# Optimization experiments

Measured on AMD Instinct MI355X. Metric: run time of the kernel, lower is better.

The kernel has to match this reference:

```python
import jax, jax.numpy as jnp
import numpy as np

B, S, E = 4, 2048, 1024


def setup_inputs() -> dict:
    key = jax.random.key(0)
    ks = jax.random.split(key, 7)
    s = 1.0 / np.sqrt(E)  # torch Linear default init scale (uniform bound)
    inp = {
        "input": jax.random.normal(ks[0], (B, S, E), dtype=jnp.float32),
        "masked": 1,
        "W_q": jax.random.uniform(ks[1], (E, E), jnp.float32, -s, s),
        "b_q": jax.random.uniform(ks[2], (E,), jnp.float32, -s, s),
        "W_k": jax.random.uniform(ks[3], (E, E), jnp.float32, -s, s),
        "b_k": jax.random.uniform(ks[4], (E,), jnp.float32, -s, s),
        "W_v": jax.random.uniform(ks[5], (E, E), jnp.float32, -s, s),
        "b_v": jax.random.uniform(ks[6], (E,), jnp.float32, -s, s),
    }
    return inp


def reference(input, masked, W_q, b_q, W_k, b_k, W_v, b_v):
    # torch.nn.Linear: y = x @ W.T + b
    q = jnp.einsum("bse,fe->bsf", input, W_q) + b_q
    k = jnp.einsum("bse,fe->bsf", input, W_k) + b_k
    v = jnp.einsum("bse,fe->bsf", input, W_v) + b_v
    d = q.shape[-1]
    scores = jnp.einsum("bqd,bkd->bqk", q, k) / jnp.sqrt(jnp.float32(d))
    if masked:
        Sq = scores.shape[1]
        causal = jnp.tril(jnp.ones((Sq, Sq), dtype=bool))  # [S,S], broadcast over batch
        scores = jnp.where(causal, scores, -jnp.inf)
    attn = jax.nn.softmax(scores, axis=-1)
    return jnp.einsum("bqk,bkd->bqd", attn, v)
```

## Files before the change

kernel.cpp:

```cpp
#include <hip/hip_runtime.h>

typedef _Float16 f16;
typedef f16 f16x8 __attribute__((ext_vector_type(8)));
typedef f16 f16x4v __attribute__((ext_vector_type(4)));
typedef f16 f16x2v __attribute__((ext_vector_type(2)));
typedef float f32x4 __attribute__((ext_vector_type(4)));

__device__ __forceinline__ void async_ld16(const void* g, void* l) {
    __builtin_amdgcn_global_load_lds(
        (const __attribute__((address_space(1))) unsigned int*)g,
        (__attribute__((address_space(3))) unsigned int*)l, 16, 0, 0);
}

#define VMC(n) asm volatile("s_waitcnt vmcnt(" #n ")" ::: "memory")
#define BAR __builtin_amdgcn_s_barrier()


#define SSTG_A(b, kh, tOff) do {                                                \
    char* d_ = (char*)smem + (b) * 32768 + (kh) * 8192 + stgBase;               \
    async_ld16(pA  + (tOff) * 64 + (kh) * 32, d_);                              \
    async_ld16(pA1 + (tOff) * 64 + (kh) * 32, d_ + 4096);                       \
} while (0)
#define SSTG_B(b, kh, tOff) do {                                                \
    char* d_ = (char*)smem + (b) * 32768 + 16384 + (kh) * 8192 + stgBase;       \
    async_ld16(pB  + (tOff) * 64 + (kh) * 32, d_);                              \
    async_ld16(pB1 + (tOff) * 64 + (kh) * 32, d_ + 4096);                       \
} while (0)
#define SRD(b, kk) do {                                                         \
    const char* sa_ = (const char*)smem + (b) * 32768 + (kk) * 8192 + aOff;     \
    _Pragma("unroll") for (int m_ = 0; m_ < 4; ++m_)                            \
        af[m_] = *(const f16x8*)(sa_ + m_ * 1024);                              \
    const char* sb_ = (const char*)smem + (b) * 32768 + 16384 + (kk) * 8192 + bOff; \
    _Pragma("unroll") for (int n_ = 0; n_ < 4; ++n_)                            \
        bf[n_] = *(const f16x8*)(sb_ + n_ * 1024);                              \
} while (0)
#define SFENCE do {                                                             \
    __builtin_amdgcn_s_barrier();                                               \
    asm volatile("s_waitcnt lgkmcnt(0)" ::: "memory");                          \
    __builtin_amdgcn_sched_barrier(0);                                          \
    __builtin_amdgcn_s_setprio(1);                                              \
    _Pragma("unroll") for (int m_ = 0; m_ < 4; ++m_)                            \
        _Pragma("unroll") for (int n_ = 0; n_ < 4; ++n_)                        \
            acc[m_][n_] = __builtin_amdgcn_mfma_f32_16x16x32_f16(af[m_], bf[n_], acc[m_][n_], 0, 0, 0); \
    __builtin_amdgcn_s_setprio(0);                                              \
} while (0)

__global__ __launch_bounds__(256, 2) void scores128(
    const f16* __restrict__ Q, const f16* __restrict__ K,
    f16* __restrict__ P, const int* __restrict__ maskedp)
{
    const int masked = *maskedp;
    const int bx = blockIdx.x, by = blockIdx.y, bz = blockIdx.z;
    if (masked && bx > by) return;
    const int mBase = by * 128, nBase = bx * 128;
    const bool diag = (masked != 0) && (bx == by);

    __shared__ __align__(16) f16 smem[32768];
    const int tid = threadIdx.x;
    const int wave = tid >> 6, lane = tid & 63;
    const int wrow = wave >> 1, wcol = wave & 1;
    const int quad = lane >> 4, l16 = lane & 15;
    const int rowLane = tid >> 2;
    const int cOff = ((tid & 3) ^ ((tid >> 3) & 3)) * 8;
    const int stgBase = wave * 1024;
    const int swz  = (quad ^ ((l16 >> 1) & 3)) * 16;
    const int aOff = (wrow * 64 + l16) * 64 + swz;
    const int bOff = (wcol * 64 + l16) * 64 + swz;

    const f16* Ab = Q + (long)bz * (2048L * 1024);
    const f16* Bb = K + (long)bz * (2048L * 1024);
    const f16* pA  = Ab + (long)(mBase + rowLane) * 1024 + cOff;
    const f16* pA1 = pA + 64 * 1024;
    const f16* pB  = Bb + (long)(nBase + rowLane) * 1024 + cOff;
    const f16* pB1 = pB + 64 * 1024;

    f32x4 acc[4][4];
#pragma unroll
    for (int m = 0; m < 4; ++m)
#pragma unroll
        for (int n = 0; n < 4; ++n) acc[m][n] = (f32x4){0.f, 0.f, 0.f, 0.f};
    f16x8 af[4], bf[4];

    SSTG_A(0, 0, 0); SSTG_B(0, 0, 0);
    SSTG_A(0, 1, 0); SSTG_B(0, 1, 0);
    SSTG_A(1, 0, 1); SSTG_B(1, 0, 1);
    VMC(4);
    BAR;

#pragma unroll 1
    for (int i = 0; i < 7; ++i) {
        SRD(0, 0); SSTG_A(1, 1, 1); SSTG_B(1, 1, 1);
        SFENCE; VMC(8); BAR;
        SRD(0, 1); SSTG_A(0, 0, 2); SSTG_B(0, 0, 2);
        SFENCE; VMC(8); BAR;
        SRD(1, 0); SSTG_A(0, 1, 2); SSTG_B(0, 1, 2);
        SFENCE; VMC(8); BAR;
        SRD(1, 1); SSTG_A(1, 0, 3); SSTG_B(1, 0, 3);
        SFENCE; VMC(8); BAR;
        pA += 128; pA1 += 128; pB += 128; pB1 += 128;
    }
    SRD(0, 0); SSTG_A(1, 1, 1); SSTG_B(1, 1, 1);
    SFENCE; VMC(8); BAR;
    SRD(0, 1);
    SFENCE; VMC(4); BAR;
    SRD(1, 0);
    SFENCE; VMC(0); BAR;
    SRD(1, 1);
    SFENCE;

    f16* Crow = P + (long)bz * (2048L * 2048);
#pragma unroll
    for (int m = 0; m < 4; ++m)
#pragma unroll
        for (int n = 0; n < 4; ++n)
#pragma unroll
            for (int r = 0; r < 4; ++r) {
                const int row = mBase + wrow * 64 + m * 16 + quad * 4 + r;
                const int col = nBase + wcol * 64 + n * 16 + l16;
                float e = __expf(acc[m][n][r] * 0.03125f);
                if (diag && col > row) e = 0.f;
                Crow[(long)row * 2048 + col] = (f16)e;
            }
}

#undef SSTG_A
#undef SSTG_B
#undef SRD
#undef SFENCE

#define QSTG_A(b, kh, tOff) do {                                                \
    char* d_ = (char*)smem + (b) * 49152 + (kh) * 8192 + stgBase;               \
    async_ld16(pA + (tOff) * 64 + (kh) * 32, d_);                               \
} while (0)
#define QSTG_B(b, kh, tOff) do {                                                \
    char* d_ = (char*)smem + (b) * 49152 + 16384 + (kh) * 16384 + stgBase;      \
    async_ld16(pB  + (tOff) * 64 + (kh) * 32, d_);                              \
    async_ld16(pB1 + (tOff) * 64 + (kh) * 32, d_ + 8192);                       \
} while (0)
#define QRD(b, kk) do {                                                         \
    const char* sa_ = (const char*)smem + (b) * 49152 + (kk) * 8192 + aOff;     \
    _Pragma("unroll") for (int m_ = 0; m_ < 4; ++m_)                            \
        af[m_] = *(const f16x8*)(sa_ + m_ * 1024);                              \
    const char* sb_ = (const char*)smem + (b) * 49152 + 16384 + (kk) * 16384 + bOff; \
    _Pragma("unroll") for (int n_ = 0; n_ < 4; ++n_)                            \
        bf[n_] = *(const f16x8*)(sb_ + n_ * 1024);                              \
} while (0)
#define QFENCE do {                                                             \
    __builtin_amdgcn_s_barrier();                                               \
    asm volatile("s_waitcnt lgkmcnt(0)" ::: "memory");                          \
    __builtin_amdgcn_sched_barrier(0);                                          \
    __builtin_amdgcn_s_setprio(1);                                              \
    _Pragma("unroll") for (int m_ = 0; m_ < 4; ++m_)                            \
        _Pragma("unroll") for (int n_ = 0; n_ < 4; ++n_)                        \
            acc[m_][n_] = __builtin_amdgcn_mfma_f32_16x16x32_f16(af[m_], bf[n_], acc[m_][n_], 0, 0, 0); \
    __builtin_amdgcn_s_setprio(0);                                              \
} while (0)

__global__ __launch_bounds__(512, 2) void qkv128(
    const f16* __restrict__ A, const f16* __restrict__ Bt,
    const float* __restrict__ b_q, const float* __restrict__ b_k,
    const float* __restrict__ b_v,
    f16* __restrict__ Q16, f16* __restrict__ K16, f16* __restrict__ Vt16)
{
    const int orig = blockIdx.x;
    const int xcd = orig & 7;
    const int s = orig >> 3;
    const int by = xcd * 8 + (s & 7);
    const int bx = s >> 3;
    const int mBase = by * 128, nBase = bx * 256;

    __shared__ __align__(16) f16 smem[49152];
    const int tid = threadIdx.x;
    const int wave = tid >> 6, lane = tid & 63;
    const int wrow = wave >> 2, wcol = wave & 3;
    const int quad = lane >> 4, l16 = lane & 15;
    const int rowLane = tid >> 2;
    const int cOff = ((tid & 3) ^ ((tid >> 3) & 3)) * 8;
    const int stgBase = wave * 1024;
    const int swz  = (quad ^ ((l16 >> 1) & 3)) * 16;
    const int aOff = (wrow * 64 + l16) * 64 + swz;
    const int bOff = (wcol * 64 + l16) * 64 + swz;

    const f16* pA  = A  + (long)(mBase + rowLane) * 1024 + cOff;
    const f16* pB  = Bt + (long)(nBase + rowLane) * 1024 + cOff;
    const f16* pB1 = pB + 128 * 1024;

    f32x4 acc[4][4];
#pragma unroll
    for (int m = 0; m < 4; ++m)
#pragma unroll
        for (int n = 0; n < 4; ++n) acc[m][n] = (f32x4){0.f, 0.f, 0.f, 0.f};
    f16x8 af[4], bf[4];

    QSTG_A(0, 0, 0); QSTG_B(0, 0, 0);
    QSTG_A(0, 1, 0); QSTG_B(0, 1, 0);
    QSTG_A(1, 0, 1); QSTG_B(1, 0, 1);
    VMC(3);
    BAR;

#pragma unroll 1
    for (int i = 0; i < 7; ++i) {
        QRD(0, 0); QSTG_A(1, 1, 1); QSTG_B(1, 1, 1);
        QFENCE; VMC(6); BAR;
        QRD(0, 1); QSTG_A(0, 0, 2); QSTG_B(0, 0, 2);
        QFENCE; VMC(6); BAR;
        QRD(1, 0); QSTG_A(0, 1, 2); QSTG_B(0, 1, 2);
        QFENCE; VMC(6); BAR;
        QRD(1, 1); QSTG_A(1, 0, 3); QSTG_B(1, 0, 3);
        QFENCE; VMC(6); BAR;
        pA += 128; pB += 128; pB1 += 128;
    }
    QRD(0, 0); QSTG_A(1, 1, 1); QSTG_B(1, 1, 1);
    QFENCE; VMC(6); BAR;
    QRD(0, 1);
    QFENCE; VMC(3); BAR;
    QRD(1, 0);
    QFENCE; VMC(0); BAR;
    QRD(1, 1);
    QFENCE;
    BAR;

    const int seg = nBase >> 10;
    const float* bs = (seg == 0) ? b_q : (seg == 1) ? b_k : b_v;
    const int lcb = (nBase & 1023) + wcol * 64;
    float bvv[4];
#pragma unroll
    for (int n = 0; n < 4; ++n) bvv[n] = bs[lcb + n * 16 + l16];

    if (seg < 2) {
        f16* dst = (seg == 0) ? Q16 : K16;
#pragma unroll
        for (int m = 0; m < 4; ++m)
#pragma unroll
            for (int n = 0; n < 4; ++n)
#pragma unroll
                for (int r = 0; r < 4; ++r) {
                    const int row = mBase + wrow * 64 + m * 16 + quad * 4 + r;
                    dst[(long)row * 1024 + lcb + n * 16 + l16] =
                        (f16)(acc[m][n][r] + bvv[n]);
                }
    } else {
        const int b = mBase >> 11;
        const int s0 = (mBase & 2047) + wrow * 64;
        const int e0 = (nBase & 1023) + wcol * 64;
        f16* epiW = smem + wave * (64 * 72);
#pragma unroll
        for (int m = 0; m < 4; ++m)
#pragma unroll
            for (int n = 0; n < 4; ++n) {
                f16x4v pk;
#pragma unroll
                for (int r = 0; r < 4; ++r)
                    pk[r] = (f16)(acc[m][n][r] + bvv[n]);
                *(f16x4v*)&epiW[(n * 16 + l16) * 72 + m * 16 + quad * 4] = pk;
            }
        asm volatile("s_waitcnt lgkmcnt(0)" ::: "memory");
#pragma unroll
        for (int it = 0; it < 8; ++it) {
            const int e = it * 8 + (lane >> 3);
            const f16x8 v = *(const f16x8*)&epiW[e * 72 + (lane & 7) * 8];
            *(f16x8*)(Vt16 + ((long)b * 1024 + e0 + e) * 2048 + s0 +
                      (lane & 7) * 8) = v;
        }
    }
}

#undef QSTG_A
#undef QSTG_B
#undef QRD
#undef QFENCE

#if defined(__has_builtin)
#if __has_builtin(__builtin_amdgcn_fdot2)
#define HAVE_FDOT2 1
#endif
#endif

#ifdef HAVE_FDOT2
#define PSUM do {                                                               \
    const f16x2v one_ = {(f16)1, (f16)1};                                       \
    _Pragma("unroll") for (int m_ = 0; m_ < 4; ++m_) {                          \
        const f16x2v* ph_ = (const f16x2v*)&af[m_];                             \
        _Pragma("unroll") for (int j_ = 0; j_ < 4; ++j_)                        \
            rs[m_] = __builtin_amdgcn_fdot2(ph_[j_], one_, rs[m_], false);      \
    }                                                                           \
} while (0)
#else
#define PSUM do {                                                               \
    _Pragma("unroll") for (int m_ = 0; m_ < 4; ++m_)                            \
        _Pragma("unroll") for (int j_ = 0; j_ < 8; ++j_)                        \
            rs[m_] += (float)af[m_][j_];                                        \
} while (0)
#endif

#define PSTG_A(b, kh, tOff) do {                                                \
    char* d_ = (char*)smem + (b) * 32768 + (kh) * 8192 + stgBase;               \
    async_ld16(pA  + (tOff) * 64 + (kh) * 32, d_);                              \
    async_ld16(pA1 + (tOff) * 64 + (kh) * 32, d_ + 4096);                       \
} while (0)
#define PSTG_B(b, kh, tOff) do {                                                \
    char* d_ = (char*)smem + (b) * 32768 + 16384 + (kh) * 8192 + stgBase;       \
    async_ld16(pB  + (tOff) * 64 + (kh) * 32, d_);                              \
    async_ld16(pB1 + (tOff) * 64 + (kh) * 32, d_ + 4096);                       \
} while (0)
#define PRD(b, kk) do {                                                         \
    const char* sa_ = (const char*)smem + (b) * 32768 + (kk) * 8192 + aOff;     \
    _Pragma("unroll") for (int m_ = 0; m_ < 4; ++m_)                            \
        af[m_] = *(const f16x8*)(sa_ + m_ * 1024);                              \
    const char* sb_ = (const char*)smem + (b) * 32768 + 16384 + (kk) * 8192 + bOff; \
    _Pragma("unroll") for (int n_ = 0; n_ < 4; ++n_)                            \
        bf[n_] = *(const f16x8*)(sb_ + n_ * 1024);                              \
} while (0)
#define PFENCE do {                                                             \
    __builtin_amdgcn_s_barrier();                                               \
    asm volatile("s_waitcnt lgkmcnt(0)" ::: "memory");                          \
    __builtin_amdgcn_sched_barrier(0);                                          \
    __builtin_amdgcn_s_setprio(1);                                              \
    _Pragma("unroll") for (int m_ = 0; m_ < 4; ++m_)                            \
        _Pragma("unroll") for (int n_ = 0; n_ < 4; ++n_)                        \
            acc[m_][n_] = __builtin_amdgcn_mfma_f32_16x16x32_f16(af[m_], bf[n_], acc[m_][n_], 0, 0, 0); \
    __builtin_amdgcn_s_setprio(0);                                              \
    PSUM;                                                                       \
} while (0)

__global__ __launch_bounds__(256, 2) void pv128(
    const f16* __restrict__ P, const f16* __restrict__ Vt,
    float* __restrict__ out, const int* __restrict__ maskedp)
{
    const int masked = *maskedp;
    const int bx = blockIdx.x, bz = blockIdx.z;
    const int by = (bz >= 2) ? blockIdx.y : (gridDim.y - 1 - blockIdx.y);
    const int mBase = by * 128, nBase = bx * 128;
    const int nIter = masked ? (by + 1) : 16;

    __shared__ __align__(16) f16 smem[32768];
    const int tid = threadIdx.x;
    const int wave = tid >> 6, lane = tid & 63;
    const int wrow = wave >> 1, wcol = wave & 1;
    const int quad = lane >> 4, l16 = lane & 15;
    const int rowLane = tid >> 2;
    const int cOff = ((tid & 3) ^ ((tid >> 3) & 3)) * 8;
    const int stgBase = wave * 1024;
    const int swz  = (quad ^ ((l16 >> 1) & 3)) * 16;
    const int aOff = (wrow * 64 + l16) * 64 + swz;
    const int bOff = (wcol * 64 + l16) * 64 + swz;

    const f16* Pb = P  + (long)bz * (2048L * 2048);
    const f16* Vb = Vt + (long)bz * (1024L * 2048);
    const f16* pA  = Pb + (long)(mBase + rowLane) * 2048 + cOff;
    const f16* pA1 = pA + 64 * 2048;
    const f16* pB  = Vb + (long)(nBase + rowLane) * 2048 + cOff;
    const f16* pB1 = pB + 64 * 2048;

    f32x4 acc[4][4];
#pragma unroll
    for (int m = 0; m < 4; ++m)
#pragma unroll
        for (int n = 0; n < 4; ++n) acc[m][n] = (f32x4){0.f, 0.f, 0.f, 0.f};
    f16x8 af[4], bf[4];
    float rs[4] = {0.f, 0.f, 0.f, 0.f};

    PSTG_A(0, 0, 0); PSTG_B(0, 0, 0);
    PSTG_A(0, 1, 0); PSTG_B(0, 1, 0);
    PSTG_A(1, 0, 1); PSTG_B(1, 0, 1);
    VMC(4);
    BAR;

#pragma unroll 1
    for (int i = 0; i < nIter - 1; ++i) {
        PRD(0, 0); PSTG_A(1, 1, 1); PSTG_B(1, 1, 1);
        PFENCE; VMC(8); BAR;
        PRD(0, 1); PSTG_A(0, 0, 2); PSTG_B(0, 0, 2);
        PFENCE; VMC(8); BAR;
        PRD(1, 0); PSTG_A(0, 1, 2); PSTG_B(0, 1, 2);
        PFENCE; VMC(8); BAR;
        PRD(1, 1); PSTG_A(1, 0, 3); PSTG_B(1, 0, 3);
        PFENCE; VMC(8); BAR;
        pA += 128; pA1 += 128; pB += 128; pB1 += 128;
    }
    PRD(0, 0); PSTG_A(1, 1, 1); PSTG_B(1, 1, 1);
    PFENCE; VMC(8); BAR;
    PRD(0, 1);
    PFENCE; VMC(4); BAR;
    PRD(1, 0);
    PFENCE; VMC(0); BAR;
    PRD(1, 1);
    PFENCE;

#pragma unroll
    for (int m = 0; m < 4; ++m) {
        rs[m] += __shfl_xor(rs[m], 16);
        rs[m] += __shfl_xor(rs[m], 32);
    }

    float* ob = out + (long)bz * (2048L * 1024);
#pragma unroll
    for (int m = 0; m < 4; ++m)
#pragma unroll
        for (int r = 0; r < 4; ++r) {
            const int row = mBase + wrow * 64 + m * 16 + quad * 4 + r;
            const float inv = 1.f / __shfl(rs[m], quad * 4 + r);
#pragma unroll
            for (int n = 0; n < 4; ++n) {
                const int col = nBase + wcol * 64 + n * 16 + l16;
                ob[(long)row * 1024 + col] = acc[m][n][r] * inv;
            }
        }
}

#undef PSTG_A
#undef PSTG_B
#undef PRD
#undef PFENCE
#undef PSUM
#undef VMC
#undef BAR

__global__ void cvt_all(const float* __restrict__ inp,
                        const float* __restrict__ W0,
                        const float* __restrict__ W1,
                        const float* __restrict__ W2,
                        f16* __restrict__ inp16, f16* __restrict__ W3)
{
    const int bxx = blockIdx.x;
    const float* src;
    f16* dst;
    int i;
    if (bxx < 8192) {
        src = inp; dst = inp16;
        i = bxx * 256 + threadIdx.x;
    } else {
        const int wb = bxx - 8192;
        const int which = wb >> 10;
        src = (which == 0) ? W0 : (which == 1) ? W1 : W2;
        dst = W3 + (long)which * 1024 * 1024;
        i = (wb & 1023) * 256 + threadIdx.x;
    }
    const float4 v = ((const float4*)src)[i];
    f16x4v o;
    o[0] = (f16)v.x; o[1] = (f16)v.y; o[2] = (f16)v.z; o[3] = (f16)v.w;
    ((f16x4v*)dst)[i] = o;
}

extern "C" void kernel_launch(void* const* d_in, const int* in_sizes, int n_in,
                              void* d_out, int out_size, void* d_ws, size_t ws_size,
                              hipStream_t stream)
{
    const float* inp = (const float*)d_in[0];
    const int* masked = (const int*)d_in[1];
    const float* Wq = (const float*)d_in[2];
    const float* bq = (const float*)d_in[3];
    const float* Wk = (const float*)d_in[4];
    const float* bk = (const float*)d_in[5];
    const float* Wv = (const float*)d_in[6];
    const float* bv = (const float*)d_in[7];
    float* out = (float*)d_out;

    const int S = 2048, E = 1024;
    const long nTok = (long)4 * S;

    char* ws = (char*)d_ws;
    f16* inp16 = (f16*)ws;   ws += nTok * E * 2;
    f16* W3    = (f16*)ws;   ws += (long)3 * E * E * 2;
    f16* Q16   = (f16*)ws;   ws += nTok * E * 2;
    f16* K16   = (f16*)ws;   ws += nTok * E * 2;
    f16* Vt16  = (f16*)ws;   ws += nTok * E * 2;
    f16* P16   = (f16*)ws;   ws += (long)4 * S * S * 2;

    cvt_all<<<dim3(8192 + 3072), dim3(256), 0, stream>>>(
        inp, Wq, Wk, Wv, inp16, W3);

    qkv128<<<dim3(768), dim3(512), 0, stream>>>(
        inp16, W3, bq, bk, bv, Q16, K16, Vt16);

    scores128<<<dim3(16, 16, 4), dim3(256), 0, stream>>>(
        Q16, K16, P16, masked);

    pv128<<<dim3(8, 16, 4), dim3(256), 0, stream>>>(
        P16, Vt16, out, masked);
}
```

Before: 226.5 us.

## Restructure QKV GEMM mainloop to three-stage ring with full 64-wide K steps

```diff
diff --git a/kernel.cpp b/kernel.cpp
--- a/kernel.cpp
+++ b/kernel.cpp
@@ -128,33 +128,41 @@
 #undef SRD
 #undef SFENCE
 
-#define QSTG_A(b, kh, tOff) do {                                                \
-    char* d_ = (char*)smem + (b) * 49152 + (kh) * 8192 + stgBase;               \
-    async_ld16(pA + (tOff) * 64 + (kh) * 32, d_);                               \
-} while (0)
-#define QSTG_B(b, kh, tOff) do {                                                \
-    char* d_ = (char*)smem + (b) * 49152 + 16384 + (kh) * 16384 + stgBase;      \
-    async_ld16(pB  + (tOff) * 64 + (kh) * 32, d_);                              \
-    async_ld16(pB1 + (tOff) * 64 + (kh) * 32, d_ + 8192);                       \
-} while (0)
-#define QRD(b, kk) do {                                                         \
-    const char* sa_ = (const char*)smem + (b) * 49152 + (kk) * 8192 + aOff;     \
-    _Pragma("unroll") for (int m_ = 0; m_ < 4; ++m_)                            \
-        af[m_] = *(const f16x8*)(sa_ + m_ * 1024);                              \
-    const char* sb_ = (const char*)smem + (b) * 49152 + 16384 + (kk) * 16384 + bOff; \
-    _Pragma("unroll") for (int n_ = 0; n_ < 4; ++n_)                            \
-        bf[n_] = *(const f16x8*)(sb_ + n_ * 1024);                              \
-} while (0)
-#define QFENCE do {                                                             \
+#define QSTG2(b, o) do {                                                        \
+    char* da_ = (char*)smem + (b) * 16384 + wave * 1024;                        \
+    async_ld16(pA + (o) * 64,      da_);                                        \
+    async_ld16(pA + (o) * 64 + 32, da_ + 8192);                                 \
+    char* db_ = (char*)smem + 49152 + (b) * 32768 + wave * 1024;                \
+    async_ld16(pB  + (o) * 64,      db_);                                       \
+    async_ld16(pB1 + (o) * 64,      db_ + 8192);                                \
+    async_ld16(pB  + (o) * 64 + 32, db_ + 16384);                               \
+    async_ld16(pB1 + (o) * 64 + 32, db_ + 16384 + 8192);                        \
+} while (0)
+#define QRD2(b) do {                                                            \
+    const char* sa_ = (const char*)smem + (b) * 16384 + aOff;                   \
+    _Pragma("unroll") for (int m_ = 0; m_ < 4; ++m_) {                          \
+        af[m_]     = *(const f16x8*)(sa_ + m_ * 1024);                          \
+        af[m_ + 4] = *(const f16x8*)(sa_ + 8192 + m_ * 1024);                   \
+    }                                                                           \
+    const char* sb_ = (const char*)smem + 49152 + (b) * 32768 + bOff;           \
+    _Pragma("unroll") for (int n_ = 0; n_ < 4; ++n_) {                          \
+        bf[n_]     = *(const f16x8*)(sb_ + n_ * 1024);                          \
+        bf[n_ + 4] = *(const f16x8*)(sb_ + 16384 + n_ * 1024);                  \
+    }                                                                           \
+} while (0)
+#define QFENCE2 do {                                                            \
     __builtin_amdgcn_s_barrier();                                               \
     asm volatile("s_waitcnt lgkmcnt(0)" ::: "memory");                          \
     __builtin_amdgcn_sched_barrier(0);                                          \
     __builtin_amdgcn_s_setprio(1);                                              \
-    _Pragma("unroll") for (int m_ = 0; m_ < 4; ++m_)                            \
-        _Pragma("unroll") for (int n_ = 0; n_ < 4; ++n_)                        \
-            acc[m_][n_] = __builtin_amdgcn_mfma_f32_16x16x32_f16(af[m_], bf[n_], acc[m_][n_], 0, 0, 0); \
+    _Pragma("unroll") for (int kk_ = 0; kk_ < 2; ++kk_)                         \
+        _Pragma("unroll") for (int m_ = 0; m_ < 4; ++m_)                        \
+            _Pragma("unroll") for (int n_ = 0; n_ < 4; ++n_)                    \
+                acc[m_][n_] = __builtin_amdgcn_mfma_f32_16x16x32_f16(           \
+                    af[kk_ * 4 + m_], bf[kk_ * 4 + n_], acc[m_][n_], 0, 0, 0);  \
     __builtin_amdgcn_s_setprio(0);                                              \
 } while (0)
+#define QT(b, b2, o2) do { QRD2(b); QSTG2(b2, o2); QFENCE2; VMC(6); BAR; } while (0)
 
 __global__ __launch_bounds__(512, 2) void qkv128(
     const f16* __restrict__ A, const f16* __restrict__ Bt,
@@ -169,14 +177,13 @@
     const int bx = s >> 3;
     const int mBase = by * 128, nBase = bx * 256;
 
-    __shared__ __align__(16) f16 smem[49152];
+    __shared__ __align__(16) f16 smem[73728];
     const int tid = threadIdx.x;
     const int wave = tid >> 6, lane = tid & 63;
     const int wrow = wave >> 2, wcol = wave & 3;
     const int quad = lane >> 4, l16 = lane & 15;
     const int rowLane = tid >> 2;
     const int cOff = ((tid & 3) ^ ((tid >> 3) & 3)) * 8;
-    const int stgBase = wave * 1024;
     const int swz  = (quad ^ ((l16 >> 1) & 3)) * 16;
     const int aOff = (wrow * 64 + l16) * 64 + swz;
     const int bOff = (wcol * 64 + l16) * 64 + swz;
@@ -190,34 +197,23 @@
     for (int m = 0; m < 4; ++m)
 #pragma unroll
         for (int n = 0; n < 4; ++n) acc[m][n] = (f32x4){0.f, 0.f, 0.f, 0.f};
-    f16x8 af[4], bf[4];
-
-    QSTG_A(0, 0, 0); QSTG_B(0, 0, 0);
-    QSTG_A(0, 1, 0); QSTG_B(0, 1, 0);
-    QSTG_A(1, 0, 1); QSTG_B(1, 0, 1);
-    VMC(3);
+    f16x8 af[8], bf[8];
+
+    QSTG2(0, 0); QSTG2(1, 1);
+    VMC(6);
     BAR;
 
 #pragma unroll 1
-    for (int i = 0; i < 7; ++i) {
-        QRD(0, 0); QSTG_A(1, 1, 1); QSTG_B(1, 1, 1);
-        QFENCE; VMC(6); BAR;
-        QRD(0, 1); QSTG_A(0, 0, 2); QSTG_B(0, 0, 2);
-        QFENCE; VMC(6); BAR;
-        QRD(1, 0); QSTG_A(0, 1, 2); QSTG_B(0, 1, 2);
-        QFENCE; VMC(6); BAR;
-        QRD(1, 1); QSTG_A(1, 0, 3); QSTG_B(1, 0, 3);
-        QFENCE; VMC(6); BAR;
-        pA += 128; pB += 128; pB1 += 128;
-    }
-    QRD(0, 0); QSTG_A(1, 1, 1); QSTG_B(1, 1, 1);
-    QFENCE; VMC(6); BAR;
-    QRD(0, 1);
-    QFENCE; VMC(3); BAR;
-    QRD(1, 0);
-    QFENCE; VMC(0); BAR;
-    QRD(1, 1);
-    QFENCE;
+    for (int g = 0; g < 4; ++g) {
+        QT(0, 2, 2);
+        QT(1, 0, 3);
+        QT(2, 1, 4);
+        pA += 192; pB += 192; pB1 += 192;
+    }
+    QT(0, 2, 2);
+    QT(1, 0, 3);
+    QRD2(2); QFENCE2; VMC(0); BAR;
+    QRD2(0); QFENCE2;
     BAR;
 
     const int seg = nBase >> 10;
@@ -265,10 +261,10 @@
     }
 }
 
-#undef QSTG_A
-#undef QSTG_B
-#undef QRD
-#undef QFENCE
+#undef QSTG2
+#undef QRD2
+#undef QFENCE2
+#undef QT
 
 #if defined(__has_builtin)
 #if __has_builtin(__builtin_amdgcn_fdot2)
```

New measurement: 227.1 us. Within noise of the previous version (+0.3%).

## Restructure QKV GEMM mainloop into three-stage ring of half-K tiles

Applied to the files above, without the earlier changes.

```diff
diff --git a/kernel.cpp b/kernel.cpp
--- a/kernel.cpp
+++ b/kernel.cpp
@@ -128,20 +128,18 @@
 #undef SRD
 #undef SFENCE
 
-#define QSTG_A(b, kh, tOff) do {                                                \
-    char* d_ = (char*)smem + (b) * 49152 + (kh) * 8192 + stgBase;               \
-    async_ld16(pA + (tOff) * 64 + (kh) * 32, d_);                               \
-} while (0)
-#define QSTG_B(b, kh, tOff) do {                                                \
-    char* d_ = (char*)smem + (b) * 49152 + 16384 + (kh) * 16384 + stgBase;      \
-    async_ld16(pB  + (tOff) * 64 + (kh) * 32, d_);                              \
-    async_ld16(pB1 + (tOff) * 64 + (kh) * 32, d_ + 8192);                       \
-} while (0)
-#define QRD(b, kk) do {                                                         \
-    const char* sa_ = (const char*)smem + (b) * 49152 + (kk) * 8192 + aOff;     \
+#define QSTG(j, o) do {                                                         \
+    char* da_ = (char*)smem + (j) * 24576 + wave * 1024;                        \
+    async_ld16(pA  + (o) * 32, da_);                                            \
+    char* db_ = (char*)smem + (j) * 24576 + 8192 + wave * 1024;                 \
+    async_ld16(pB  + (o) * 32, db_);                                            \
+    async_ld16(pB1 + (o) * 32, db_ + 8192);                                     \
+} while (0)
+#define QRD(j) do {                                                             \
+    const char* sa_ = (const char*)smem + (j) * 24576 + aOff;                   \
     _Pragma("unroll") for (int m_ = 0; m_ < 4; ++m_)                            \
         af[m_] = *(const f16x8*)(sa_ + m_ * 1024);                              \
-    const char* sb_ = (const char*)smem + (b) * 49152 + 16384 + (kk) * 16384 + bOff; \
+    const char* sb_ = (const char*)smem + (j) * 24576 + 8192 + bOff;            \
     _Pragma("unroll") for (int n_ = 0; n_ < 4; ++n_)                            \
         bf[n_] = *(const f16x8*)(sb_ + n_ * 1024);                              \
 } while (0)
@@ -155,6 +153,7 @@
             acc[m_][n_] = __builtin_amdgcn_mfma_f32_16x16x32_f16(af[m_], bf[n_], acc[m_][n_], 0, 0, 0); \
     __builtin_amdgcn_s_setprio(0);                                              \
 } while (0)
+#define QT(j, j2, o2) do { QRD(j); QSTG(j2, o2); QFENCE; VMC(3); BAR; } while (0)
 
 __global__ __launch_bounds__(512, 2) void qkv128(
     const f16* __restrict__ A, const f16* __restrict__ Bt,
@@ -169,14 +168,13 @@
     const int bx = s >> 3;
     const int mBase = by * 128, nBase = bx * 256;
 
-    __shared__ __align__(16) f16 smem[49152];
+    __shared__ __align__(16) f16 smem[36864];
     const int tid = threadIdx.x;
     const int wave = tid >> 6, lane = tid & 63;
     const int wrow = wave >> 2, wcol = wave & 3;
     const int quad = lane >> 4, l16 = lane & 15;
     const int rowLane = tid >> 2;
     const int cOff = ((tid & 3) ^ ((tid >> 3) & 3)) * 8;
-    const int stgBase = wave * 1024;
     const int swz  = (quad ^ ((l16 >> 1) & 3)) * 16;
     const int aOff = (wrow * 64 + l16) * 64 + swz;
     const int bOff = (wcol * 64 + l16) * 64 + swz;
@@ -192,32 +190,19 @@
         for (int n = 0; n < 4; ++n) acc[m][n] = (f32x4){0.f, 0.f, 0.f, 0.f};
     f16x8 af[4], bf[4];
 
-    QSTG_A(0, 0, 0); QSTG_B(0, 0, 0);
-    QSTG_A(0, 1, 0); QSTG_B(0, 1, 0);
-    QSTG_A(1, 0, 1); QSTG_B(1, 0, 1);
+    QSTG(0, 0); QSTG(1, 1);
     VMC(3);
     BAR;
 
 #pragma unroll 1
-    for (int i = 0; i < 7; ++i) {
-        QRD(0, 0); QSTG_A(1, 1, 1); QSTG_B(1, 1, 1);
-        QFENCE; VMC(6); BAR;
-        QRD(0, 1); QSTG_A(0, 0, 2); QSTG_B(0, 0, 2);
-        QFENCE; VMC(6); BAR;
-        QRD(1, 0); QSTG_A(0, 1, 2); QSTG_B(0, 1, 2);
-        QFENCE; VMC(6); BAR;
-        QRD(1, 1); QSTG_A(1, 0, 3); QSTG_B(1, 0, 3);
-        QFENCE; VMC(6); BAR;
-        pA += 128; pB += 128; pB1 += 128;
-    }
-    QRD(0, 0); QSTG_A(1, 1, 1); QSTG_B(1, 1, 1);
-    QFENCE; VMC(6); BAR;
-    QRD(0, 1);
-    QFENCE; VMC(3); BAR;
-    QRD(1, 0);
-    QFENCE; VMC(0); BAR;
-    QRD(1, 1);
-    QFENCE;
+    for (int g = 0; g < 10; ++g) {
+        QT(0, 2, 2);
+        QT(1, 0, 3);
+        QT(2, 1, 4);
+        pA += 96; pB += 96; pB1 += 96;
+    }
+    QRD(0); QFENCE; VMC(0); BAR;
+    QRD(1); QFENCE;
     BAR;
 
     const int seg = nBase >> 10;
@@ -265,10 +250,10 @@
     }
 }
 
-#undef QSTG_A
-#undef QSTG_B
+#undef QSTG
 #undef QRD
 #undef QFENCE
+#undef QT
 
 #if defined(__has_builtin)
 #if __has_builtin(__builtin_amdgcn_fdot2)
```

After: 233.0 us. 1.03x slower.
